# Kernel optimization log

Measured on AMD Instinct MI355X. Metric: run time of the kernel, lower is better.

## Reference

```python
import jax, jax.numpy as jnp
import numpy as np

NUM_NODES = 50000
NUM_EDGES = 800000
IN_F = 64
OUT_F = 64
EDGE_DIM = 16
NUM_GRAPHS = 64
T = 1.0
NEG_SLOPE = 0.2


def setup_inputs() -> dict:
    key = jax.random.key(0)
    k = jax.random.split(key, 6)
    x = jax.random.normal(k[0], (NUM_NODES, IN_F), dtype=jnp.float32)
    edge_index = jax.random.randint(k[1], (2, NUM_EDGES), 0, NUM_NODES, dtype=jnp.int32)
    edge_attr = jax.random.normal(k[2], (NUM_EDGES, EDGE_DIM), dtype=jnp.float32)
    batch_id = jnp.sort(jax.random.randint(k[3], (NUM_NODES,), 0, NUM_GRAPHS, dtype=jnp.int32))
    # Xavier-ish scaled params
    W = jax.random.normal(k[4], (IN_F, OUT_F), dtype=jnp.float32) * (1.0 / np.sqrt(IN_F))
    a = jax.random.normal(k[5], (2 * OUT_F + EDGE_DIM, 1), dtype=jnp.float32) * 0.1
    return {"x": x, "edge_index": edge_index, "edge_attr": edge_attr,
            "batch_id": batch_id, "W": W, "a": a}


def reference(x, edge_index, edge_attr, batch_id, W, a):
    num_nodes = x.shape[0]
    src0, dst0 = edge_index[0], edge_index[1]
    loop = jnp.arange(num_nodes, dtype=src0.dtype)
    # undirected: add reverse edges; then self loops
    src = jnp.concatenate([src0, dst0, loop])
    dst = jnp.concatenate([dst0, src0, loop])

    xt = x @ W  # [N, F]
    a_src = a[:OUT_F, 0]
    a_dst = a[OUT_F:2 * OUT_F, 0]
    a_edge = a[2 * OUT_F:, 0]
    # per-node attention contributions (equivalent to concat([h_src,h_dst,e]) @ a)
    s_node = xt @ a_src  # [N]
    d_node = xt @ a_dst  # [N]
    e_contrib = edge_attr @ a_edge  # [E]
    # self-loop edge_attr is zeros -> contribution 0
    e_all = jnp.concatenate([e_contrib, e_contrib, jnp.zeros((num_nodes,), xt.dtype)])

    logits = jax.nn.leaky_relu(s_node[src] + d_node[dst] + e_all, NEG_SLOPE) / T

    # segment softmax over dst
    m = jax.ops.segment_max(logits, dst, num_segments=num_nodes)
    z = jnp.exp(logits - m[dst])
    denom = jax.ops.segment_sum(z, dst, num_segments=num_nodes)
    att = z / denom[dst]  # [E_total]

    h_src = xt[src]  # [E_total, F]
    out = jax.ops.segment_sum(att[:, None] * h_src, dst, num_segments=num_nodes)
    return out
```

## Files before the change

### kernel.cpp

```cpp
#include <hip/hip_runtime.h>
#include <hip/hip_fp16.h>

#define N_NODES 50000
#define N_EDGES 800000
#define ETOT    (2 * N_EDGES + N_NODES)
#define F       64
#define NEG_SLOPE 0.2f
#define SCAN_B  1024
#define NB      ((N_NODES + SCAN_B - 1) / SCAN_B)

#define RSPLIT  4
#define NRANGE  (N_NODES / RSPLIT)
#define CCHUNK  64
#define EPC     (N_EDGES / CCHUNK)
#define BLD     1024

#define XT_TASKS (N_NODES / 16)

typedef _Float16 half8 __attribute__((ext_vector_type(8)));
typedef float    f32x4 __attribute__((ext_vector_type(4)));

__device__ __forceinline__ float leaky(float v) {
    return (v > 0.f) ? v : NEG_SLOPE * v;
}
__device__ __forceinline__ unsigned int pack_entry(int src, float w) {
    __half h = __float2half(w);
    return (unsigned int)(unsigned short)src |
           ((unsigned int)__half_as_ushort(h) << 16);
}
__device__ __forceinline__ void cr_decode(int bid, int& c, int& r) {
    const int m = bid & 7;
    r = m >> 1;
    c = ((bid >> 3) << 1) | (m & 1);
}

__global__ void __launch_bounds__(256) k_xt(const float* __restrict__ x,
                                            const float* __restrict__ W,
                                            const float* __restrict__ a,
                                            __half* __restrict__ xt,
                                            float2* __restrict__ sd) {
    const int lane = threadIdx.x & 63;
    const int task = blockIdx.x * 4 + (threadIdx.x >> 6);
    if (task >= XT_TASKS) return;
    const int n0  = task * 16;
    const int r16 = lane & 15;
    const int kb  = lane >> 4;

    half8 bf[4][2];
#pragma unroll
    for (int c = 0; c < 4; ++c)
#pragma unroll
        for (int ks = 0; ks < 2; ++ks) {
            const float* wp = W + (size_t)(ks * 32 + kb * 8) * 64 + c * 16 + r16;
#pragma unroll
            for (int j = 0; j < 8; ++j) bf[c][ks][j] = (_Float16)wp[j * 64];
        }

    half8 af[2];
#pragma unroll
    for (int ks = 0; ks < 2; ++ks) {
        const float* xp = x + (size_t)(n0 + r16) * F + ks * 32 + kb * 8;
        const float4 v0 = *(const float4*)xp;
        const float4 v1 = *(const float4*)(xp + 4);
        af[ks][0] = (_Float16)v0.x; af[ks][1] = (_Float16)v0.y;
        af[ks][2] = (_Float16)v0.z; af[ks][3] = (_Float16)v0.w;
        af[ks][4] = (_Float16)v1.x; af[ks][5] = (_Float16)v1.y;
        af[ks][6] = (_Float16)v1.z; af[ks][7] = (_Float16)v1.w;
    }

    f32x4 acc[4];
#pragma unroll
    for (int c = 0; c < 4; ++c) {
        acc[c] = (f32x4){0.f, 0.f, 0.f, 0.f};
        acc[c] = __builtin_amdgcn_mfma_f32_16x16x32_f16(af[0], bf[c][0], acc[c], 0, 0, 0);
        acc[c] = __builtin_amdgcn_mfma_f32_16x16x32_f16(af[1], bf[c][1], acc[c], 0, 0, 0);
    }

    float ps[4] = {0.f, 0.f, 0.f, 0.f};
    float pd[4] = {0.f, 0.f, 0.f, 0.f};
#pragma unroll
    for (int c = 0; c < 4; ++c) {
        const float as_ = a[c * 16 + r16];
        const float ad_ = a[64 + c * 16 + r16];
#pragma unroll
        for (int r = 0; r < 4; ++r) {
            const float v = acc[c][r];
            const int n = n0 + kb * 4 + r;
            xt[(size_t)n * F + c * 16 + r16] = __float2half(v);
            ps[r] = fmaf(v, as_, ps[r]);
            pd[r] = fmaf(v, ad_, pd[r]);
        }
    }
#pragma unroll
    for (int r = 0; r < 4; ++r) {
#pragma unroll
        for (int off = 1; off <= 8; off <<= 1) {
            ps[r] += __shfl_xor(ps[r], off);
            pd[r] += __shfl_xor(pd[r], off);
        }
    }
    if (r16 == 0) {
#pragma unroll
        for (int r = 0; r < 4; ++r) sd[n0 + kb * 4 + r] = make_float2(ps[r], pd[r]);
    }
}

__global__ void __launch_bounds__(BLD) k_histA(const int* __restrict__ srcs,
                                               const int* __restrict__ dsts,
                                               const float* __restrict__ ea,
                                               const float* __restrict__ a,
                                               __half* __restrict__ ec,
                                               unsigned short* __restrict__ cnt) {
    __shared__ int h[NRANGE];
    int c, r;
    cr_decode(blockIdx.x, c, r);
    const int nbase = r * NRANGE;
    for (int i = threadIdx.x; i < NRANGE; i += BLD) h[i] = 0;
    __syncthreads();
    const int e0 = c * EPC;
    for (int i = e0 + threadIdx.x; i < e0 + EPC; i += BLD) {
        const int d = dsts[i] - nbase;
        if ((unsigned)d < NRANGE) atomicAdd(&h[d], 1);
        const int s = srcs[i] - nbase;
        if ((unsigned)s < NRANGE) atomicAdd(&h[s], 1);
    }
    const int eq0 = e0 + (r * EPC) / RSPLIT;
    const int eq1 = e0 + ((r + 1) * EPC) / RSPLIT;
    for (int i = eq0 + threadIdx.x; i < eq1; i += BLD) {
        const float4* p = (const float4*)(ea + (size_t)i * 16);
        float acc = 0.f;
#pragma unroll
        for (int k = 0; k < 4; ++k) {
            float4 v = p[k];
            acc += v.x * a[128 + k * 4 + 0] + v.y * a[128 + k * 4 + 1] +
                   v.z * a[128 + k * 4 + 2] + v.w * a[128 + k * 4 + 3];
        }
        ec[i] = __float2half(acc);
    }
    __syncthreads();
    unsigned short* o = cnt + (size_t)c * N_NODES + nbase;
    for (int i = threadIdx.x; i < NRANGE; i += BLD) o[i] = (unsigned short)h[i];
}

__global__ void k_scanA(unsigned short* __restrict__ cnt, int* __restrict__ part,
                        int* __restrict__ bsum) {
    __shared__ int wtot[16];
    __shared__ int wexc[16];
    const int tid = threadIdx.x, lane = tid & 63, wid = tid >> 6;
    const int i = blockIdx.x * SCAN_B + tid;
    int v = 0;
    if (i < N_NODES) {
        int run = 0;
#pragma unroll 8
        for (int c = 0; c < CCHUNK; ++c) {
            const int t = cnt[(size_t)c * N_NODES + i];
            cnt[(size_t)c * N_NODES + i] = (unsigned short)run;
            run += t;
        }
        v = run + 1;
    }
    int s = v;
#pragma unroll
    for (int off = 1; off < 64; off <<= 1) { int u = __shfl_up(s, off); if (lane >= off) s += u; }
    if (lane == 63) wtot[wid] = s;
    __syncthreads();
    if (tid == 0) { int run = 0; for (int w = 0; w < 16; ++w) { wexc[w] = run; run += wtot[w]; } bsum[blockIdx.x] = run; }
    __syncthreads();
    if (i < N_NODES) part[i] = wexc[wid] + s - v;
}

__global__ void k_scanC(const int* __restrict__ part, const int* __restrict__ bsum,
                        const float2* __restrict__ sd, int* __restrict__ offs,
                        unsigned int* __restrict__ csr) {
    __shared__ int base;
    if (threadIdx.x < 64) {
        const int lane = threadIdx.x;
        const int v = (lane < NB) ? bsum[lane] : 0;
        int s = v;
#pragma unroll
        for (int off = 1; off < 64; off <<= 1) { int u = __shfl_up(s, off); if (lane >= off) s += u; }
        if (lane == (int)blockIdx.x) base = s - v;
    }
    __syncthreads();
    const int i = blockIdx.x * SCAN_B + threadIdx.x;
    if (i < N_NODES) {
        const int o = part[i] + base;
        offs[i] = o;
        const float2 v = sd[i];
        csr[o] = pack_entry(i, __expf(leaky(v.x + v.y)));
    }
    if (i == 0) offs[N_NODES] = ETOT;
}

__global__ void __launch_bounds__(BLD) k_scatter(const int* __restrict__ srcs,
                                                 const int* __restrict__ dsts,
                                                 const float2* __restrict__ sd,
                                                 const __half* __restrict__ ec,
                                                 const unsigned short* __restrict__ cnt,
                                                 const int* __restrict__ offs,
                                                 unsigned int* __restrict__ csr) {
    __shared__ int cur[NRANGE];
    int c, r;
    cr_decode(blockIdx.x, c, r);
    const int nbase = r * NRANGE;
    const unsigned short* cslice = cnt + (size_t)c * N_NODES + nbase;
    const int* oslice = offs + nbase;
    for (int i = threadIdx.x; i < NRANGE; i += BLD) cur[i] = oslice[i] + 1 + cslice[i];
    __syncthreads();
    const int e0 = c * EPC;
    for (int i = e0 + threadIdx.x; i < e0 + EPC; i += BLD) {
        const int s = srcs[i], d = dsts[i];
        const int dl = d - nbase, sl = s - nbase;
        const bool din = (unsigned)dl < NRANGE;
        const bool sin_ = (unsigned)sl < NRANGE;
        if (!din && !sin_) continue;
        const float e = __half2float(ec[i]);
        const float2 ss = sd[s], dd = sd[d];
        if (din) {
            const int pos = atomicAdd(&cur[dl], 1);
            csr[pos] = pack_entry(s, __expf(leaky(ss.x + dd.y + e)));
        }
        if (sin_) {
            const int pos = atomicAdd(&cur[sl], 1);
            csr[pos] = pack_entry(d, __expf(leaky(dd.x + ss.y + e)));
        }
    }
}

__global__ void __launch_bounds__(256) k_node(const int* __restrict__ offs,
                                              const unsigned int* __restrict__ csr,
                                              const __half* __restrict__ xt,
                                              float* __restrict__ out) {
    const int node = (blockIdx.x * blockDim.x + threadIdx.x) >> 6;
    const int lane = threadIdx.x & 63;
    if (node >= N_NODES) return;
    const int beg = offs[node], end = offs[node + 1];
    const int jg = lane >> 3;
    const int fc = lane & 7;
    float acc[8] = {0.f, 0.f, 0.f, 0.f, 0.f, 0.f, 0.f, 0.f};
    float sum = 0.f;
    for (int j = beg + jg; j < end; j += 8) {
        const unsigned int ent = csr[j];
        const int   src = (int)(ent & 0xFFFFu);
        const float w   = __half2float(__ushort_as_half((unsigned short)(ent >> 16)));
        sum += w;
        const uint4 hv = *(const uint4*)(xt + (size_t)src * F + fc * 8);
        const __half2* hp = (const __half2*)&hv;
#pragma unroll
        for (int k = 0; k < 4; ++k) {
            const float2 f = __half22float2(hp[k]);
            acc[2 * k]     += w * f.x;
            acc[2 * k + 1] += w * f.y;
        }
    }
#pragma unroll
    for (int off = 8; off <= 32; off <<= 1) {
        sum += __shfl_xor(sum, off);
#pragma unroll
        for (int k = 0; k < 8; ++k) acc[k] += __shfl_xor(acc[k], off);
    }
    if (jg == 0) {
        const float inv = 1.0f / sum;
        float4* op = (float4*)(out + (size_t)node * F + fc * 8);
        op[0] = make_float4(acc[0] * inv, acc[1] * inv, acc[2] * inv, acc[3] * inv);
        op[1] = make_float4(acc[4] * inv, acc[5] * inv, acc[6] * inv, acc[7] * inv);
    }
}

extern "C" void kernel_launch(void* const* d_in, const int* in_sizes, int n_in,
                              void* d_out, int out_size, void* d_ws, size_t ws_size,
                              hipStream_t stream) {
    const float* x    = (const float*)d_in[0];
    const int*   ei   = (const int*)d_in[1];
    const float* ea   = (const float*)d_in[2];
    const float* W    = (const float*)d_in[4];
    const float* a    = (const float*)d_in[5];
    float* out = (float*)d_out;

    const int* srcs = ei;
    const int* dsts = ei + N_EDGES;

    char* ws = (char*)d_ws;
    size_t off = 0;
    auto alloc = [&](size_t bytes) { void* p = ws + off; off = (off + bytes + 255) & ~(size_t)255; return p; };
    __half*         xt   = (__half*)alloc((size_t)N_NODES * F * 2);
    float2*         sd   = (float2*)alloc((size_t)N_NODES * 8);
    __half*         ec   = (__half*)alloc((size_t)N_EDGES * 2);
    unsigned short* cnt  = (unsigned short*)alloc((size_t)CCHUNK * N_NODES * 2);
    int*            part = (int*)alloc((size_t)N_NODES * 4);
    int*            bsum = (int*)alloc((size_t)NB * 4);
    int*            offs = (int*)alloc((size_t)(N_NODES + 1) * 4);
    unsigned int*   csr  = (unsigned int*)alloc((size_t)ETOT * 4);

    k_xt<<<(XT_TASKS + 3) / 4, 256, 0, stream>>>(x, W, a, xt, sd);
    k_histA<<<CCHUNK * RSPLIT, BLD, 0, stream>>>(srcs, dsts, ea, a, ec, cnt);
    k_scanA<<<NB, SCAN_B, 0, stream>>>(cnt, part, bsum);
    k_scanC<<<NB, SCAN_B, 0, stream>>>(part, bsum, sd, offs, csr);
    k_scatter<<<CCHUNK * RSPLIT, BLD, 0, stream>>>(srcs, dsts, sd, ec, cnt, offs, csr);
    k_node<<<((size_t)N_NODES * 64 + 255) / 256, 256, 0, stream>>>(offs, csr, xt, out);
}
```

Before: 109.7 us.

## Merge xt and histogram kernels; fuse scan into single-pass decoupled lookback

Combines the node transform (MFMA) and the edge histogram into one launch, with block ranges split by role, so both run concurrently. The two-kernel scan is replaced by a single kernel in which each block publishes its aggregate through a flag word and reads its predecessors' aggregates. This removes two launches and the intermediate part/bsum buffers. In exchange, the xt blocks now carry the large shared histogram allocation and 1024-thread blocks. The lookback spin relies on all 49 scan blocks being co-resident, which holds on this GPU.

```diff
diff --git a/kernel.cpp b/kernel.cpp
--- a/kernel.cpp
+++ b/kernel.cpp
@@ -7,7 +7,7 @@
 #define F       64
 #define NEG_SLOPE 0.2f
 #define SCAN_B  1024
-#define NB      ((N_NODES + SCAN_B - 1) / SCAN_B)
+#define NB_S    ((N_NODES + SCAN_B - 1) / SCAN_B)
 
 #define RSPLIT  4
 #define NRANGE  (N_NODES / RSPLIT)
@@ -15,7 +15,9 @@
 #define EPC     (N_EDGES / CCHUNK)
 #define BLD     1024
 
-#define XT_TASKS (N_NODES / 16)
+#define XT_TASKS  (N_NODES / 16)
+#define HIST_BLKS (CCHUNK * RSPLIT)
+#define XT_BLKS   ((XT_TASKS + 15) / 16)
 
 typedef _Float16 half8 __attribute__((ext_vector_type(8)));
 typedef float    f32x4 __attribute__((ext_vector_type(4)));
@@ -34,120 +36,128 @@
     c = ((bid >> 3) << 1) | (m & 1);
 }
 
-__global__ void __launch_bounds__(256) k_xt(const float* __restrict__ x,
-                                            const float* __restrict__ W,
-                                            const float* __restrict__ a,
-                                            __half* __restrict__ xt,
-                                            float2* __restrict__ sd) {
-    const int lane = threadIdx.x & 63;
-    const int task = blockIdx.x * 4 + (threadIdx.x >> 6);
-    if (task >= XT_TASKS) return;
-    const int n0  = task * 16;
-    const int r16 = lane & 15;
-    const int kb  = lane >> 4;
-
-    half8 bf[4][2];
-#pragma unroll
-    for (int c = 0; c < 4; ++c)
+__global__ void __launch_bounds__(BLD) k_front(const float* __restrict__ x,
+                                               const float* __restrict__ W,
+                                               const float* __restrict__ a,
+                                               const float* __restrict__ ea,
+                                               const int* __restrict__ srcs,
+                                               const int* __restrict__ dsts,
+                                               __half* __restrict__ xt,
+                                               float2* __restrict__ sd,
+                                               __half* __restrict__ ec,
+                                               unsigned short* __restrict__ cnt,
+                                               unsigned long long* __restrict__ state) {
+    __shared__ int h[NRANGE];
+    if (blockIdx.x == 0 && threadIdx.x < NB_S) state[threadIdx.x] = 0ull;
+
+    if (blockIdx.x < HIST_BLKS) {
+        int c, r;
+        cr_decode(blockIdx.x, c, r);
+        const int nbase = r * NRANGE;
+        for (int i = threadIdx.x; i < NRANGE; i += BLD) h[i] = 0;
+        __syncthreads();
+        const int e0 = c * EPC;
+        for (int i = e0 + threadIdx.x; i < e0 + EPC; i += BLD) {
+            const int d = dsts[i] - nbase;
+            if ((unsigned)d < NRANGE) atomicAdd(&h[d], 1);
+            const int s = srcs[i] - nbase;
+            if ((unsigned)s < NRANGE) atomicAdd(&h[s], 1);
+        }
+        const int eq0 = e0 + (r * EPC) / RSPLIT;
+        const int eq1 = e0 + ((r + 1) * EPC) / RSPLIT;
+        for (int i = eq0 + threadIdx.x; i < eq1; i += BLD) {
+            const float4* p = (const float4*)(ea + (size_t)i * 16);
+            float acc = 0.f;
+#pragma unroll
+            for (int k = 0; k < 4; ++k) {
+                float4 v = p[k];
+                acc += v.x * a[128 + k * 4 + 0] + v.y * a[128 + k * 4 + 1] +
+                       v.z * a[128 + k * 4 + 2] + v.w * a[128 + k * 4 + 3];
+            }
+            ec[i] = __float2half(acc);
+        }
+        __syncthreads();
+        unsigned short* o = cnt + (size_t)c * N_NODES + nbase;
+        for (int i = threadIdx.x; i < NRANGE; i += BLD) o[i] = (unsigned short)h[i];
+    } else {
+        const int lane = threadIdx.x & 63;
+        const int task = (blockIdx.x - HIST_BLKS) * 16 + (threadIdx.x >> 6);
+        if (task >= XT_TASKS) return;
+        const int n0  = task * 16;
+        const int r16 = lane & 15;
+        const int kb  = lane >> 4;
+
+        half8 bf[4][2];
+#pragma unroll
+        for (int c = 0; c < 4; ++c)
+#pragma unroll
+            for (int ks = 0; ks < 2; ++ks) {
+                const float* wp = W + (size_t)(ks * 32 + kb * 8) * 64 + c * 16 + r16;
+#pragma unroll
+                for (int j = 0; j < 8; ++j) bf[c][ks][j] = (_Float16)wp[j * 64];
+            }
+
+        half8 af[2];
 #pragma unroll
         for (int ks = 0; ks < 2; ++ks) {
-            const float* wp = W + (size_t)(ks * 32 + kb * 8) * 64 + c * 16 + r16;
-#pragma unroll
-            for (int j = 0; j < 8; ++j) bf[c][ks][j] = (_Float16)wp[j * 64];
-        }
-
-    half8 af[2];
-#pragma unroll
-    for (int ks = 0; ks < 2; ++ks) {
-        const float* xp = x + (size_t)(n0 + r16) * F + ks * 32 + kb * 8;
-        const float4 v0 = *(const float4*)xp;
-        const float4 v1 = *(const float4*)(xp + 4);
-        af[ks][0] = (_Float16)v0.x; af[ks][1] = (_Float16)v0.y;
-        af[ks][2] = (_Float16)v0.z; af[ks][3] = (_Float16)v0.w;
-        af[ks][4] = (_Float16)v1.x; af[ks][5] = (_Float16)v1.y;
-        af[ks][6] = (_Float16)v1.z; af[ks][7] = (_Float16)v1.w;
-    }
-
-    f32x4 acc[4];
-#pragma unroll
-    for (int c = 0; c < 4; ++c) {
-        acc[c] = (f32x4){0.f, 0.f, 0.f, 0.f};
-        acc[c] = __builtin_amdgcn_mfma_f32_16x16x32_f16(af[0], bf[c][0], acc[c], 0, 0, 0);
-        acc[c] = __builtin_amdgcn_mfma_f32_16x16x32_f16(af[1], bf[c][1], acc[c], 0, 0, 0);
-    }
-
-    float ps[4] = {0.f, 0.f, 0.f, 0.f};
-    float pd[4] = {0.f, 0.f, 0.f, 0.f};
-#pragma unroll
-    for (int c = 0; c < 4; ++c) {
-        const float as_ = a[c * 16 + r16];
-        const float ad_ = a[64 + c * 16 + r16];
+            const float* xp = x + (size_t)(n0 + r16) * F + ks * 32 + kb * 8;
+            const float4 v0 = *(const float4*)xp;
+            const float4 v1 = *(const float4*)(xp + 4);
+            af[ks][0] = (_Float16)v0.x; af[ks][1] = (_Float16)v0.y;
+            af[ks][2] = (_Float16)v0.z; af[ks][3] = (_Float16)v0.w;
+            af[ks][4] = (_Float16)v1.x; af[ks][5] = (_Float16)v1.y;
+            af[ks][6] = (_Float16)v1.z; af[ks][7] = (_Float16)v1.w;
+        }
+
+        f32x4 acc[4];
+#pragma unroll
+        for (int c = 0; c < 4; ++c) {
+            acc[c] = (f32x4){0.f, 0.f, 0.f, 0.f};
+            acc[c] = __builtin_amdgcn_mfma_f32_16x16x32_f16(af[0], bf[c][0], acc[c], 0, 0, 0);
+            acc[c] = __builtin_amdgcn_mfma_f32_16x16x32_f16(af[1], bf[c][1], acc[c], 0, 0, 0);
+        }
+
+        float ps[4] = {0.f, 0.f, 0.f, 0.f};
+        float pd[4] = {0.f, 0.f, 0.f, 0.f};
+#pragma unroll
+        for (int c = 0; c < 4; ++c) {
+            const float as_ = a[c * 16 + r16];
+            const float ad_ = a[64 + c * 16 + r16];
+#pragma unroll
+            for (int r = 0; r < 4; ++r) {
+                const float v = acc[c][r];
+                const int n = n0 + kb * 4 + r;
+                xt[(size_t)n * F + c * 16 + r16] = __float2half(v);
+                ps[r] = fmaf(v, as_, ps[r]);
+                pd[r] = fmaf(v, ad_, pd[r]);
+            }
+        }
 #pragma unroll
         for (int r = 0; r < 4; ++r) {
-            const float v = acc[c][r];
-            const int n = n0 + kb * 4 + r;
-            xt[(size_t)n * F + c * 16 + r16] = __float2half(v);
-            ps[r] = fmaf(v, as_, ps[r]);
-            pd[r] = fmaf(v, ad_, pd[r]);
-        }
-    }
-#pragma unroll
-    for (int r = 0; r < 4; ++r) {
-#pragma unroll
-        for (int off = 1; off <= 8; off <<= 1) {
-            ps[r] += __shfl_xor(ps[r], off);
-            pd[r] += __shfl_xor(pd[r], off);
-        }
-    }
-    if (r16 == 0) {
-#pragma unroll
-        for (int r = 0; r < 4; ++r) sd[n0 + kb * 4 + r] = make_float2(ps[r], pd[r]);
-    }
-}
-
-__global__ void __launch_bounds__(BLD) k_histA(const int* __restrict__ srcs,
-                                               const int* __restrict__ dsts,
-                                               const float* __restrict__ ea,
-                                               const float* __restrict__ a,
-                                               __half* __restrict__ ec,
-                                               unsigned short* __restrict__ cnt) {
-    __shared__ int h[NRANGE];
-    int c, r;
-    cr_decode(blockIdx.x, c, r);
-    const int nbase = r * NRANGE;
-    for (int i = threadIdx.x; i < NRANGE; i += BLD) h[i] = 0;
-    __syncthreads();
-    const int e0 = c * EPC;
-    for (int i = e0 + threadIdx.x; i < e0 + EPC; i += BLD) {
-        const int d = dsts[i] - nbase;
-        if ((unsigned)d < NRANGE) atomicAdd(&h[d], 1);
-        const int s = srcs[i] - nbase;
-        if ((unsigned)s < NRANGE) atomicAdd(&h[s], 1);
-    }
-    const int eq0 = e0 + (r * EPC) / RSPLIT;
-    const int eq1 = e0 + ((r + 1) * EPC) / RSPLIT;
-    for (int i = eq0 + threadIdx.x; i < eq1; i += BLD) {
-        const float4* p = (const float4*)(ea + (size_t)i * 16);
-        float acc = 0.f;
-#pragma unroll
-        for (int k = 0; k < 4; ++k) {
-            float4 v = p[k];
-            acc += v.x * a[128 + k * 4 + 0] + v.y * a[128 + k * 4 + 1] +
-                   v.z * a[128 + k * 4 + 2] + v.w * a[128 + k * 4 + 3];
-        }
-        ec[i] = __float2half(acc);
-    }
-    __syncthreads();
-    unsigned short* o = cnt + (size_t)c * N_NODES + nbase;
-    for (int i = threadIdx.x; i < NRANGE; i += BLD) o[i] = (unsigned short)h[i];
-}
-
-__global__ void k_scanA(unsigned short* __restrict__ cnt, int* __restrict__ part,
-                        int* __restrict__ bsum) {
+#pragma unroll
+            for (int off = 1; off <= 8; off <<= 1) {
+                ps[r] += __shfl_xor(ps[r], off);
+                pd[r] += __shfl_xor(pd[r], off);
+            }
+        }
+        if (r16 == 0) {
+#pragma unroll
+            for (int r = 0; r < 4; ++r) sd[n0 + kb * 4 + r] = make_float2(ps[r], pd[r]);
+        }
+    }
+}
+
+__global__ void k_scan(unsigned short* __restrict__ cnt,
+                       const float2* __restrict__ sd,
+                       int* __restrict__ offs,
+                       unsigned int* __restrict__ csr,
+                       unsigned long long* __restrict__ state) {
     __shared__ int wtot[16];
     __shared__ int wexc[16];
+    __shared__ int sbase;
     const int tid = threadIdx.x, lane = tid & 63, wid = tid >> 6;
-    const int i = blockIdx.x * SCAN_B + tid;
+    const int bid = blockIdx.x;
+    const int i = bid * SCAN_B + tid;
     int v = 0;
     if (i < N_NODES) {
         int run = 0;
@@ -164,32 +174,35 @@
     for (int off = 1; off < 64; off <<= 1) { int u = __shfl_up(s, off); if (lane >= off) s += u; }
     if (lane == 63) wtot[wid] = s;
     __syncthreads();
-    if (tid == 0) { int run = 0; for (int w = 0; w < 16; ++w) { wexc[w] = run; run += wtot[w]; } bsum[blockIdx.x] = run; }
+    if (tid == 0) {
+        int run = 0;
+        for (int w = 0; w < 16; ++w) { wexc[w] = run; run += wtot[w]; }
+        __hip_atomic_store(&state[bid], (1ull << 32) | (unsigned)run,
+                           __ATOMIC_RELEASE, __HIP_MEMORY_SCOPE_AGENT);
+    }
     __syncthreads();
-    if (i < N_NODES) part[i] = wexc[wid] + s - v;
-}
-
-__global__ void k_scanC(const int* __restrict__ part, const int* __restrict__ bsum,
-                        const float2* __restrict__ sd, int* __restrict__ offs,
-                        unsigned int* __restrict__ csr) {
-    __shared__ int base;
-    if (threadIdx.x < 64) {
-        const int lane = threadIdx.x;
-        const int v = (lane < NB) ? bsum[lane] : 0;
-        int s = v;
-#pragma unroll
-        for (int off = 1; off < 64; off <<= 1) { int u = __shfl_up(s, off); if (lane >= off) s += u; }
-        if (lane == (int)blockIdx.x) base = s - v;
+    if (wid == 0) {
+        int ag = 0;
+        if (lane < bid) {
+            unsigned long long st;
+            do {
+                st = __hip_atomic_load(&state[lane], __ATOMIC_ACQUIRE,
+                                       __HIP_MEMORY_SCOPE_AGENT);
+            } while (!(st >> 32));
+            ag = (int)(st & 0xFFFFFFFFull);
+        }
+#pragma unroll
+        for (int off = 32; off >= 1; off >>= 1) ag += __shfl_xor(ag, off);
+        if (lane == 0) sbase = ag;
     }
     __syncthreads();
-    const int i = blockIdx.x * SCAN_B + threadIdx.x;
     if (i < N_NODES) {
-        const int o = part[i] + base;
+        const int o = sbase + wexc[wid] + s - v;
         offs[i] = o;
-        const float2 v = sd[i];
-        csr[o] = pack_entry(i, __expf(leaky(v.x + v.y)));
-    }
-    if (i == 0) offs[N_NODES] = ETOT;
+        const float2 t = sd[i];
+        csr[o] = pack_entry(i, __expf(leaky(t.x + t.y)));
+        if (i == 0) offs[N_NODES] = ETOT;
+    }
 }
 
 __global__ void __launch_bounds__(BLD) k_scatter(const int* __restrict__ srcs,
@@ -283,19 +296,16 @@
     char* ws = (char*)d_ws;
     size_t off = 0;
     auto alloc = [&](size_t bytes) { void* p = ws + off; off = (off + bytes + 255) & ~(size_t)255; return p; };
-    __half*         xt   = (__half*)alloc((size_t)N_NODES * F * 2);
-    float2*         sd   = (float2*)alloc((size_t)N_NODES * 8);
-    __half*         ec   = (__half*)alloc((size_t)N_EDGES * 2);
-    unsigned short* cnt  = (unsigned short*)alloc((size_t)CCHUNK * N_NODES * 2);
-    int*            part = (int*)alloc((size_t)N_NODES * 4);
-    int*            bsum = (int*)alloc((size_t)NB * 4);
-    int*            offs = (int*)alloc((size_t)(N_NODES + 1) * 4);
-    unsigned int*   csr  = (unsigned int*)alloc((size_t)ETOT * 4);
-
-    k_xt<<<(XT_TASKS + 3) / 4, 256, 0, stream>>>(x, W, a, xt, sd);
-    k_histA<<<CCHUNK * RSPLIT, BLD, 0, stream>>>(srcs, dsts, ea, a, ec, cnt);
-    k_scanA<<<NB, SCAN_B, 0, stream>>>(cnt, part, bsum);
-    k_scanC<<<NB, SCAN_B, 0, stream>>>(part, bsum, sd, offs, csr);
-    k_scatter<<<CCHUNK * RSPLIT, BLD, 0, stream>>>(srcs, dsts, sd, ec, cnt, offs, csr);
+    __half*             xt    = (__half*)alloc((size_t)N_NODES * F * 2);
+    float2*             sd    = (float2*)alloc((size_t)N_NODES * 8);
+    __half*             ec    = (__half*)alloc((size_t)N_EDGES * 2);
+    unsigned short*     cnt   = (unsigned short*)alloc((size_t)CCHUNK * N_NODES * 2);
+    int*                offs  = (int*)alloc((size_t)(N_NODES + 1) * 4);
+    unsigned int*       csr   = (unsigned int*)alloc((size_t)ETOT * 4);
+    unsigned long long* state = (unsigned long long*)alloc((size_t)NB_S * 8);
+
+    k_front<<<HIST_BLKS + XT_BLKS, BLD, 0, stream>>>(x, W, a, ea, srcs, dsts, xt, sd, ec, cnt, state);
+    k_scan<<<NB_S, SCAN_B, 0, stream>>>(cnt, sd, offs, csr, state);
+    k_scatter<<<HIST_BLKS, BLD, 0, stream>>>(srcs, dsts, sd, ec, cnt, offs, csr);
     k_node<<<((size_t)N_NODES * 64 + 255) / 256, 256, 0, stream>>>(offs, csr, xt, out);
 }
```

After: 105.0 us. 4.3% less time.
